# Kernel optimization log

Measured on AMD Instinct MI355X. Metric: run time of the kernel, lower is better.

The kernel has to match this reference:

```python
import jax, jax.numpy as jnp
import numpy as np

TAU = 0.5  # matches init_kwargs tau
EPS = 1e-8  # torch CosineSimilarity eps


def setup_inputs() -> dict:
    key = jax.random.key(0)
    k1, k2 = jax.random.split(key)
    B, D = 4096, 256
    return {
        "z_orig": jax.random.normal(k1, (B, D), dtype=jnp.float32),
        "z_augment": jax.random.normal(k2, (B, D), dtype=jnp.float32),
    }


def reference(z_orig, z_augment):
    B = z_orig.shape[0]
    N = 2 * B
    # collect_z = cat([z_augment, z_orig])  -> [2B, D]
    z = jnp.concatenate([z_augment, z_orig], axis=0)
    # cosine similarity matrix via L2 normalize + matmul
    zn = z / jnp.maximum(jnp.linalg.norm(z, axis=-1, keepdims=True), EPS)
    S = zn @ zn.T  # [2B, 2B]
    # positives: diag offsets +B and -B
    pos = jnp.concatenate([jnp.diagonal(S, B), jnp.diagonal(S, -B)])[:, None]  # [2B, 1]
    # negatives: everything except main diag and the +/-B diagonals.
    # Static indices (shape-dependent only), computed in numpy at trace time.
    mask = ~((np.eye(N, k=B) + np.eye(N, k=-B) + np.eye(N)).astype(bool))
    flat_idx = jnp.asarray(np.nonzero(mask.reshape(-1))[0])  # [2B*(2B-2)]
    neg = S.reshape(-1)[flat_idx].reshape(N, N - 2)  # row-major order matches torch boolean mask
    logits = jnp.concatenate([pos, neg], axis=1) / TAU  # [2B, 2B-1]
    # CrossEntropy with label 0 for every row, reduction='sum', then / 2B
    loss = -jax.nn.log_softmax(logits, axis=-1)[:, 0]
    return jnp.sum(loss) / N
```

## Files before the change

### kernel.cpp

```cpp
#include <hip/hip_runtime.h>
#include <hip/hip_bf16.h>

typedef __attribute__((ext_vector_type(4))) float f32x4;
typedef __attribute__((ext_vector_type(2))) long longx2;

#define N_ROWS 8192
#define B_HALF 4096
#define NUT   2080
#define EXP2C 2.885390081777927f

#define WS_ZN       0
#define WS_ROWACC   2097152
#define WS_POS      2129920
#define WS_DIAG     2162688
#define WS_ACC      2195456
#define WS_CNT      2195460

__device__ __forceinline__ float fexp2(float x) {
#if __has_builtin(__builtin_amdgcn_exp2f)
    return __builtin_amdgcn_exp2f(x);
#else
    return exp2f(x);
#endif
}

__device__ __forceinline__ void async_copy16(const void* g, void* l) {
    __builtin_amdgcn_global_load_lds(
        (const __attribute__((address_space(1))) unsigned int*)g,
        (__attribute__((address_space(3))) unsigned int*)l,
        16, 0, 0);
}

__global__ __launch_bounds__(256) void normalize_k(
    const float* __restrict__ z_orig, const float* __restrict__ z_aug,
    unsigned char* __restrict__ zn, float* __restrict__ rowAcc,
    float* __restrict__ accum, unsigned int* __restrict__ cnt)
{
    if (blockIdx.x == 0 && threadIdx.x == 0) { *accum = 0.0f; *cnt = 0u; }
    const int row  = blockIdx.x * 4 + (threadIdx.x >> 6);
    const int lane = threadIdx.x & 63;
    if (lane == 0) rowAcc[row] = 0.0f;
    const float* src = (row < B_HALF) ? (z_aug  + (size_t)row * 256)
                                      : (z_orig + (size_t)(row - B_HALF) * 256);
    float4 v = ((const float4*)src)[lane];
    float ss = v.x*v.x + v.y*v.y + v.z*v.z + v.w*v.w;
    #pragma unroll
    for (int m = 1; m < 64; m <<= 1) ss += __shfl_xor(ss, m);
    float inv = 1.0f / fmaxf(sqrtf(ss), 1e-8f);
    int pk = 0;
    pk = __builtin_amdgcn_cvt_pk_fp8_f32(v.x * inv, v.y * inv, pk, false);
    pk = __builtin_amdgcn_cvt_pk_fp8_f32(v.z * inv, v.w * inv, pk, true);
    const int o4 = (((lane >> 1) & 3) << 6) | ((lane >> 3) << 3) | ((lane & 1) << 2);
    *(int*)(zn + (size_t)row * 256 + o4) = pk;
}

__global__ __launch_bounds__(256) void tile_k(
    const unsigned char* __restrict__ zn,
    float* __restrict__ rowAcc,
    float* __restrict__ posv,
    float* __restrict__ diagE)
{
    __shared__ unsigned char As[128 * 256];
    __shared__ unsigned char Bs[128 * 256];

    const int bid = blockIdx.x;
    int rb = (int)((129.0f - sqrtf(16641.0f - 8.0f * (float)bid)) * 0.5f);
    rb = rb < 0 ? 0 : (rb > 63 ? 63 : rb);
    while ((rb + 1) * (129 - (rb + 1)) / 2 <= bid) ++rb;
    while (rb * (129 - rb) / 2 > bid) --rb;
    const int cb = rb + (bid - rb * (129 - rb) / 2);

    const int t      = threadIdx.x;
    const int lane   = t & 63;
    const int w      = t >> 6;
    const int wy     = w >> 1;
    const int wx     = w & 1;
    const int lane15 = lane & 15;
    const int quad   = lane >> 4;
    const int rowBase = rb * 128;
    const int colBase = cb * 128;

    const int rloc = t >> 4;
    const int q16  = (((t & 15) ^ (rloc & 7)) << 4);
    const int ldsW = w * 1024;

    const unsigned char* gA = zn + (size_t)rowBase * 256;
    #pragma unroll
    for (int s = 0; s < 8; ++s)
        async_copy16(gA + (size_t)(s * 16 + rloc) * 256 + q16, As + s * 4096 + ldsW);
    if (cb != rb) {
        const unsigned char* gB = zn + (size_t)colBase * 256;
        #pragma unroll
        for (int s = 0; s < 8; ++s)
            async_copy16(gB + (size_t)(s * 16 + rloc) * 256 + q16, Bs + s * 4096 + ldsW);
    }
    const unsigned char* Bbase = (cb == rb) ? As : Bs;

    f32x4 acc[4][4];
    #pragma unroll
    for (int i = 0; i < 4; ++i)
        #pragma unroll
        for (int j = 0; j < 4; ++j)
            acc[i][j] = (f32x4){0.f, 0.f, 0.f, 0.f};

    const int h  = lane15 & 7;
    const int rA = (wy * 64 + lane15) * 256;
    const int rB = (wx * 64 + lane15) * 256;

    __syncthreads();

    #pragma unroll
    for (int t4 = 0; t4 < 4; ++t4) {
        const int off = (((4 * quad + t4) ^ h) << 4);
        longx2 a[4], b[4];
        #pragma unroll
        for (int mi = 0; mi < 4; ++mi)
            a[mi] = *(const longx2*)(As + rA + mi * 4096 + off);
        #pragma unroll
        for (int ni = 0; ni < 4; ++ni)
            b[ni] = *(const longx2*)(Bbase + rB + ni * 4096 + off);
        #pragma unroll
        for (int mi = 0; mi < 4; ++mi)
            #pragma unroll
            for (int ni = 0; ni < 4; ++ni)
                acc[mi][ni] = __builtin_amdgcn_mfma_f32_16x16x32_fp8_fp8(
                                  a[mi].x, b[ni].x, acc[mi][ni], 0, 0, 0);
        #pragma unroll
        for (int mi = 0; mi < 4; ++mi)
            #pragma unroll
            for (int ni = 0; ni < 4; ++ni)
                acc[mi][ni] = __builtin_amdgcn_mfma_f32_16x16x32_fp8_fp8(
                                  a[mi].y, b[ni].y, acc[mi][ni], 0, 0, 0);
    }

    const bool diagLane = (wy == wx) && ((lane15 >> 2) == quad);
    const int  rsel = lane15 & 3;
    if (cb == rb && diagLane) {
        #pragma unroll
        for (int mi = 0; mi < 4; ++mi) {
            int grow = rowBase + wy * 64 + mi * 16 + lane15;
            diagE[grow] = fexp2(acc[mi][mi][rsel] * EXP2C);
        }
    }
    if (cb == rb + 32 && diagLane) {
        #pragma unroll
        for (int mi = 0; mi < 4; ++mi) {
            int grow = rowBase + wy * 64 + mi * 16 + lane15;
            float v = acc[mi][mi][rsel];
            posv[grow] = v;
            posv[grow + B_HALF] = v;
        }
    }

    #pragma unroll
    for (int mi = 0; mi < 4; ++mi)
        #pragma unroll
        for (int ni = 0; ni < 4; ++ni)
            #pragma unroll
            for (int r = 0; r < 4; ++r)
                acc[mi][ni][r] = fexp2(acc[mi][ni][r] * EXP2C);

    #pragma unroll
    for (int mi = 0; mi < 4; ++mi)
        #pragma unroll
        for (int r = 0; r < 4; ++r) {
            float s = acc[mi][0][r] + acc[mi][1][r] + acc[mi][2][r] + acc[mi][3][r];
            s += __shfl_xor(s, 1);
            s += __shfl_xor(s, 2);
            s += __shfl_xor(s, 4);
            s += __shfl_xor(s, 8);
            if (lane15 == 0)
                atomicAdd(&rowAcc[rowBase + wy * 64 + mi * 16 + quad * 4 + r], s);
        }

    if (cb != rb) {
        #pragma unroll
        for (int ni = 0; ni < 4; ++ni) {
            float s = 0.0f;
            #pragma unroll
            for (int mi = 0; mi < 4; ++mi)
                s += acc[mi][ni][0] + acc[mi][ni][1] + acc[mi][ni][2] + acc[mi][ni][3];
            s += __shfl_xor(s, 16);
            s += __shfl_xor(s, 32);
            if (quad == 0)
                atomicAdd(&rowAcc[colBase + wx * 64 + ni * 16 + lane15], s);
        }
    }
}

__global__ __launch_bounds__(256) void loss_k(
    const float* __restrict__ rowAcc, const float* __restrict__ posv,
    const float* __restrict__ diagE, float* __restrict__ accum,
    unsigned int* __restrict__ cnt, float* __restrict__ out)
{
    const int i = blockIdx.x * 256 + threadIdx.x;
    float s = rowAcc[i] - diagE[i];
    float loss = __logf(s) - 2.0f * posv[i];

    #pragma unroll
    for (int m = 1; m < 64; m <<= 1) loss += __shfl_xor(loss, m);
    __shared__ float red[4];
    if ((threadIdx.x & 63) == 0) red[threadIdx.x >> 6] = loss;
    __syncthreads();
    if (threadIdx.x == 0) {
        float bs = red[0] + red[1] + red[2] + red[3];
        atomicAdd(accum, bs);
        __threadfence();
        unsigned int old = atomicAdd(cnt, 1u);
        if (old == 31u) {
            __threadfence();
            float total = atomicAdd(accum, 0.0f);
            out[0] = total * (1.0f / (float)N_ROWS);
        }
    }
}

extern "C" void kernel_launch(void* const* d_in, const int* in_sizes, int n_in,
                              void* d_out, int out_size, void* d_ws, size_t ws_size,
                              hipStream_t stream) {
    const float* z_orig = (const float*)d_in[0];
    const float* z_aug  = (const float*)d_in[1];
    char* ws = (char*)d_ws;
    unsigned char* zn   = (unsigned char*)(ws + WS_ZN);
    float* rowAcc       = (float*)(ws + WS_ROWACC);
    float* posv         = (float*)(ws + WS_POS);
    float* diagE        = (float*)(ws + WS_DIAG);
    float* accum        = (float*)(ws + WS_ACC);
    unsigned int* cnt   = (unsigned int*)(ws + WS_CNT);

    normalize_k<<<N_ROWS / 4, 256, 0, stream>>>(z_orig, z_aug, zn, rowAcc, accum, cnt);
    tile_k<<<NUT, 256, 0, stream>>>(zn, rowAcc, posv, diagE);
    loss_k<<<N_ROWS / 256, 256, 0, stream>>>(rowAcc, posv, diagE, accum, cnt,
                                             (float*)d_out);
}
```

Before: 108.4 us.

## Store fp8 normalized rows in MFMA fragment layout and load directly from global

The normalize kernel now writes fp8 rows in a tiled layout that matches the MFMA operand fragments, so each lane of the tile kernel reads its 16-byte operands straight from global memory (through cache) instead of staging 64KB per block in LDS. This removes LDS allocation and the block barrier, and with launch bounds of 3 allows more resident blocks per CU. In exchange, operand reuse across waves now relies on L1/L2 rather than shared memory, and the K loop is no longer unrolled, which exposes global load latency per step.

```diff
diff --git a/kernel.cpp b/kernel.cpp
--- a/kernel.cpp
+++ b/kernel.cpp
@@ -22,13 +22,6 @@
 #else
     return exp2f(x);
 #endif
-}
-
-__device__ __forceinline__ void async_copy16(const void* g, void* l) {
-    __builtin_amdgcn_global_load_lds(
-        (const __attribute__((address_space(1))) unsigned int*)g,
-        (__attribute__((address_space(3))) unsigned int*)l,
-        16, 0, 0);
 }
 
 __global__ __launch_bounds__(256) void normalize_k(
@@ -50,19 +43,18 @@
     int pk = 0;
     pk = __builtin_amdgcn_cvt_pk_fp8_f32(v.x * inv, v.y * inv, pk, false);
     pk = __builtin_amdgcn_cvt_pk_fp8_f32(v.z * inv, v.w * inv, pk, true);
-    const int o4 = (((lane >> 1) & 3) << 6) | ((lane >> 3) << 3) | ((lane & 1) << 2);
-    *(int*)(zn + (size_t)row * 256 + o4) = pk;
-}
-
-__global__ __launch_bounds__(256) void tile_k(
+    const int addr = ((row >> 4) << 12) | ((lane >> 4) << 10) | ((row & 15) << 6)
+                   | (((lane >> 1) & 3) << 4) | (((lane >> 3) & 1) << 3)
+                   | ((lane & 1) << 2);
+    *(int*)(zn + addr) = pk;
+}
+
+__global__ __launch_bounds__(256, 3) void tile_k(
     const unsigned char* __restrict__ zn,
     float* __restrict__ rowAcc,
     float* __restrict__ posv,
     float* __restrict__ diagE)
 {
-    __shared__ unsigned char As[128 * 256];
-    __shared__ unsigned char Bs[128 * 256];
-
     const int bid = blockIdx.x;
     int rb = (int)((129.0f - sqrtf(16641.0f - 8.0f * (float)bid)) * 0.5f);
     rb = rb < 0 ? 0 : (rb > 63 ? 63 : rb);
@@ -80,21 +72,9 @@
     const int rowBase = rb * 128;
     const int colBase = cb * 128;
 
-    const int rloc = t >> 4;
-    const int q16  = (((t & 15) ^ (rloc & 7)) << 4);
-    const int ldsW = w * 1024;
-
-    const unsigned char* gA = zn + (size_t)rowBase * 256;
-    #pragma unroll
-    for (int s = 0; s < 8; ++s)
-        async_copy16(gA + (size_t)(s * 16 + rloc) * 256 + q16, As + s * 4096 + ldsW);
-    if (cb != rb) {
-        const unsigned char* gB = zn + (size_t)colBase * 256;
-        #pragma unroll
-        for (int s = 0; s < 8; ++s)
-            async_copy16(gB + (size_t)(s * 16 + rloc) * 256 + q16, Bs + s * 4096 + ldsW);
-    }
-    const unsigned char* Bbase = (cb == rb) ? As : Bs;
+    const int laneOff = lane15 * 64 + quad * 16;
+    const unsigned char* gA = zn + (size_t)(rb * 8 + wy * 4) * 4096 + laneOff;
+    const unsigned char* gB = zn + (size_t)(cb * 8 + wx * 4) * 4096 + laneOff;
 
     f32x4 acc[4][4];
     #pragma unroll
@@ -103,22 +83,15 @@
         for (int j = 0; j < 4; ++j)
             acc[i][j] = (f32x4){0.f, 0.f, 0.f, 0.f};
 
-    const int h  = lane15 & 7;
-    const int rA = (wy * 64 + lane15) * 256;
-    const int rB = (wx * 64 + lane15) * 256;
-
-    __syncthreads();
-
-    #pragma unroll
+    #pragma unroll 1
     for (int t4 = 0; t4 < 4; ++t4) {
-        const int off = (((4 * quad + t4) ^ h) << 4);
         longx2 a[4], b[4];
         #pragma unroll
         for (int mi = 0; mi < 4; ++mi)
-            a[mi] = *(const longx2*)(As + rA + mi * 4096 + off);
+            a[mi] = *(const longx2*)(gA + mi * 4096 + t4 * 1024);
         #pragma unroll
         for (int ni = 0; ni < 4; ++ni)
-            b[ni] = *(const longx2*)(Bbase + rB + ni * 4096 + off);
+            b[ni] = *(const longx2*)(gB + ni * 4096 + t4 * 1024);
         #pragma unroll
         for (int mi = 0; mi < 4; ++mi)
             #pragma unroll
```

Result: faster. 100.7 us (-7.2%).
